# Kernel optimization log

Measured on AMD Instinct MI355X. Metric: run time of the kernel, lower is better.

The kernel has to match this reference:

```python
import jax, jax.numpy as jnp
import numpy as np
from jax import lax

N = 5000          # num atoms
E = 4             # num edge types
DIM_H = 128
VOCAB = 100       # num_atoms_vocab; embedding table has VOCAB+1 rows
T = 4             # max_time_steps


def setup_inputs() -> dict:
    key = jax.random.key(0)
    k1, k2, k3, k4 = jax.random.split(key, 4)
    atom_arr = jax.random.randint(k1, (N,), 0, VOCAB, dtype=jnp.int64 if jax.config.read('jax_enable_x64') else jnp.int32)
    adjs = jax.random.randint(k2, (E, N, N), 0, 2, dtype=jnp.int32)
    # learned parameters
    embedding = jax.random.normal(k3, (VOCAB + 1, DIM_H), dtype=jnp.float32) * 0.05
    limit = float(np.sqrt(6.0 / (DIM_H + DIM_H)))  # glorot uniform
    H_edges = jax.random.uniform(k4, (E, DIM_H, DIM_H), minval=-limit, maxval=limit, dtype=jnp.float32)
    return {
        "atom_arr": atom_arr,
        "adjs": adjs,
        "max_time_steps": T,
        "embedding": embedding,
        "H_edges": H_edges,
    }


def reference(atom_arr, adjs, max_time_steps, embedding, H_edges):
    # h_v^0 = embedding lookup, [N, H]
    h0 = embedding[atom_arr]
    # adjacency mask as float, [E, N, N]
    A = (adjs == 1).astype(h0.dtype)

    def step(h, _):
        # original: for each node v, edge type e: H_e @ sum_{u: adj[e,v,u]==1} h_u
        agg = jnp.einsum('evu,uh->evh', A, h)          # neighbor sum per edge type
        msg = jnp.einsum('eij,evj->vi', H_edges, agg)  # edge-type transform + sum over e
        h_new = jax.nn.sigmoid(h + msg)
        return h_new, h_new

    _, h_all = lax.scan(step, h0, None, length=max_time_steps)
    return h_all  # [T, N, H]
```

## Files before the change

kernel.cpp:

```cpp
#include <hip/hip_runtime.h>

#define NROW 5000
#define NPAD 5120
#define KPAD 5120
#define KW   80
#define KC   80
#define KZ   4
#define KCQ  20
#define HDIM 128
#define FXS  4194304.0f
#define PART ((size_t)4 * NROW * HDIM)

typedef _Float16 f16x8 __attribute__((ext_vector_type(8)));
typedef float f32x16 __attribute__((ext_vector_type(16)));

__device__ __forceinline__ unsigned short f2h_int(int v) {
    union { _Float16 h; unsigned short u; } c;
    c.h = (_Float16)(float)v;
    return c.u;
}
__device__ __forceinline__ void fx_digits(float h, unsigned short& d1, unsigned short& d0) {
    int q = (int)rintf(h * FXS);
    d1 = f2h_int(q >> 11);
    d0 = f2h_int(q & 2047);
}

__device__ __forceinline__ size_t ht_idx(int pl, int kc, int i, int kin) {
    return (((size_t)pl * KC + kc) * HDIM + i) * 64 + kin;
}

__global__ __launch_bounds__(256) void prep_atom_kernel(const unsigned int* __restrict__ atomw,
                                                        int* __restrict__ atomIdx) {
    __shared__ int s_is64;
    if (threadIdx.x == 0) {
        bool all0 = true, anynz = false;
        for (int j = 0; j < 64; ++j) {
            unsigned lo = atomw[2 * j], hi = atomw[2 * j + 1];
            all0 = all0 && (hi == 0u);
            anynz = anynz || (lo != 0u);
        }
        s_is64 = (all0 && anynz) ? 1 : 0;
    }
    __syncthreads();
    int v = blockIdx.x * 256 + threadIdx.x;
    if (v < NROW) atomIdx[v] = s_is64 ? (int)atomw[2 * v] : (int)atomw[v];
}

__global__ __launch_bounds__(256) void prep_pack_kernel(const int* __restrict__ adjs,
                                                        unsigned long long* __restrict__ packed) {
    const int er = blockIdx.x;
    const int e = er / NPAD;
    const int r = er - e * NPAD;
    const int wave = threadIdx.x >> 6;
    const int lane = threadIdx.x & 63;
    const int* rowp = adjs + ((size_t)e * NROW + r) * NROW;
    unsigned long long* outp = packed + ((size_t)e * NPAD + r) * KW;
    const bool rok = (r < NROW);
    for (int c = wave; c < KW; c += 4) {
        int u = c * 64 + lane;
        int val = (rok && u < NROW) ? rowp[u] : 0;
        unsigned long long m = __ballot(val == 1);
        if (lane == 0) outp[c] = m;
    }
}

__global__ __launch_bounds__(256) void prep_h0T_kernel(const int* __restrict__ atomIdx,
                                                       const float* __restrict__ emb,
                                                       unsigned short* __restrict__ hTt) {
    const int i = blockIdx.y;
    const int v = blockIdx.x * 256 + threadIdx.x;
    float val = 0.f;
    if (v < NROW) val = emb[(size_t)atomIdx[v] * HDIM + i];
    unsigned short d1, d0;
    fx_digits(val, d1, d0);
    hTt[ht_idx(0, v >> 6, i, v & 63)] = d1;
    hTt[ht_idx(1, v >> 6, i, v & 63)] = d0;
}

__global__ __launch_bounds__(256) void prep_h0f_kernel(const int* __restrict__ atomIdx,
                                                       const float* __restrict__ emb,
                                                       float* __restrict__ h) {
    int idx = blockIdx.x * 256 + threadIdx.x;
    int v = idx >> 7, i = idx & 127;
    h[idx] = emb[(size_t)atomIdx[v] * HDIM + i];
}

__global__ __launch_bounds__(256) void prep_Ht_kernel(const float* __restrict__ H,
                                                      float* __restrict__ Htr) {
    int idx = blockIdx.x * 256 + threadIdx.x;
    int e = idx >> 14;
    int j = (idx >> 7) & 127;
    int i = idx & 127;
    Htr[idx] = H[((size_t)e * HDIM + i) * HDIM + j];
}

__global__ __launch_bounds__(256, 2) void gemm1_kernel(const uint2* __restrict__ packed2,
                                                       const unsigned short* __restrict__ hTt,
                                                       float* __restrict__ agg) {
    const int m0 = blockIdx.x * 128;
    const int e = blockIdx.y;
    const int kz = blockIdx.z;
    const int tid = threadIdx.x;
    const int lane = tid & 63;
    const int wave = tid >> 6;
    const int l31 = lane & 31;
    const int l1 = lane >> 5;
    const int sh2 = l1 * 8;
    const int cb = wave * 32;
    const int col = cb + l31;

    f32x16 acc[2][4];
#pragma unroll
    for (int pl = 0; pl < 2; ++pl)
#pragma unroll
        for (int mt = 0; mt < 4; ++mt) acc[pl][mt] = (f32x16)(0.f);

    const uint2* ap[4];
#pragma unroll
    for (int mt = 0; mt < 4; ++mt)
        ap[mt] = packed2 + ((size_t)e * NPAD + (m0 + mt * 32 + l31)) * KW;

    const _Float16* bbase = (const _Float16*)hTt;
    const int kc0 = kz * KCQ;
    const _Float16* bp[2];
#pragma unroll
    for (int pl = 0; pl < 2; ++pl)
        bp[pl] = bbase + (((size_t)pl * KC + kc0) * HDIM + col) * 64 + sh2;

    for (int kc = kc0; kc < kc0 + KCQ; ++kc) {
        uint2 aw[4];
#pragma unroll
        for (int mt = 0; mt < 4; ++mt) aw[mt] = ap[mt][kc];
        const size_t coff = (size_t)(kc - kc0) * (HDIM * 64);

        f16x8 bf[2][4];
#pragma unroll
        for (int pl = 0; pl < 2; ++pl)
#pragma unroll
            for (int kk = 0; kk < 4; ++kk)
                bf[pl][kk] = *(const f16x8*)(bp[pl] + coff + kk * 16);

#pragma unroll
        for (int kk = 0; kk < 4; ++kk) {
#pragma unroll
            for (int mt = 0; mt < 4; ++mt) {
                unsigned int w = (kk < 2) ? aw[mt].x : aw[mt].y;
                unsigned int b = (w >> ((kk & 1) * 16 + sh2)) & 0xFFu;
                unsigned int y = b | (b << 15);
                union { unsigned int u[4]; f16x8 h; } A;
#pragma unroll
                for (int q = 0; q < 4; ++q)
                    A.u[q] = ((y >> (2 * q)) & 0x00010001u) * 0x3C00u;
#pragma unroll
                for (int pl = 0; pl < 2; ++pl)
                    acc[pl][mt] = __builtin_amdgcn_mfma_f32_32x32x16_f16(
                        A.h, bf[pl][kk], acc[pl][mt], 0, 0, 0);
            }
        }
    }

    float* aggz = agg + (size_t)kz * PART;
#pragma unroll
    for (int mt = 0; mt < 4; ++mt)
#pragma unroll
        for (int reg = 0; reg < 16; ++reg) {
            int row = (reg & 3) + 8 * (reg >> 2) + 4 * l1;
            int v = m0 + mt * 32 + row;
            if (v < NROW) {
                double d = (double)acc[0][mt][reg] * 2048.0 + (double)acc[1][mt][reg];
                aggz[((size_t)e * NROW + v) * HDIM + col] = (float)(d * (1.0 / 4194304.0));
            }
        }
}

__global__ __launch_bounds__(256) void gemm2_kernel(const float* __restrict__ agg,
                                                    const float* __restrict__ Htr,
                                                    float* __restrict__ h,
                                                    float* __restrict__ outp,
                                                    unsigned short* __restrict__ hTt) {
    __shared__ float aggs[16][512];
    __shared__ unsigned short hs[2][128][16];
    const int v0 = blockIdx.x * 16;
    const int tid = threadIdx.x;

#pragma unroll
    for (int it = 0; it < 8; ++it) {
        int idx = it * 256 + tid;
        int vv = idx >> 7;
        int ej = (idx & 127) * 4;
        int e = ej >> 7, j = ej & 127;
        int v = v0 + vv;
        float4 val = make_float4(0.f, 0.f, 0.f, 0.f);
        if (v < NROW) {
            size_t o = ((size_t)e * NROW + v) * HDIM + j;
            float4 a0 = *(const float4*)&agg[o];
            float4 a1 = *(const float4*)&agg[PART + o];
            float4 a2 = *(const float4*)&agg[2 * PART + o];
            float4 a3 = *(const float4*)&agg[3 * PART + o];
            val = make_float4((a0.x + a1.x) + (a2.x + a3.x), (a0.y + a1.y) + (a2.y + a3.y),
                              (a0.z + a1.z) + (a2.z + a3.z), (a0.w + a1.w) + (a2.w + a3.w));
        }
        *(float4*)&aggs[vv][ej] = val;
    }
    __syncthreads();

    const int i = tid & 127;
    const int vg = tid >> 7;
    float m4[8][4];
#pragma unroll
    for (int vv = 0; vv < 8; ++vv)
#pragma unroll
        for (int k = 0; k < 4; ++k) m4[vv][k] = 0.f;

    for (int c = 0; c < 512; c += 4) {
        float w0 = Htr[(size_t)(c + 0) * HDIM + i];
        float w1 = Htr[(size_t)(c + 1) * HDIM + i];
        float w2 = Htr[(size_t)(c + 2) * HDIM + i];
        float w3 = Htr[(size_t)(c + 3) * HDIM + i];
#pragma unroll
        for (int vv = 0; vv < 8; ++vv) {
            const float4 a = *(const float4*)&aggs[vg * 8 + vv][c];
            m4[vv][0] += a.x * w0;
            m4[vv][1] += a.y * w1;
            m4[vv][2] += a.z * w2;
            m4[vv][3] += a.w * w3;
        }
    }

#pragma unroll
    for (int vv = 0; vv < 8; ++vv) {
        int v = v0 + vg * 8 + vv;
        unsigned short d1 = 0, d0 = 0;
        if (v < NROW) {
            size_t o = (size_t)v * HDIM + i;
            float msg = (m4[vv][0] + m4[vv][1]) + (m4[vv][2] + m4[vv][3]);
            float x = h[o] + msg;
            float s = 1.0f / (1.0f + expf(-x));
            outp[o] = s;
            h[o] = s;
            fx_digits(s, d1, d0);
        }
        hs[0][i][vg * 8 + vv] = d1;
        hs[1][i][vg * 8 + vv] = d0;
    }
    __syncthreads();
    if (tid < 128) {
#pragma unroll
        for (int pl = 0; pl < 2; ++pl) {
            uint4* d = (uint4*)&hTt[ht_idx(pl, v0 >> 6, tid, v0 & 63)];
            const uint4* sp = (const uint4*)&hs[pl][tid][0];
            d[0] = sp[0];
            d[1] = sp[1];
        }
    }
}

extern "C" void kernel_launch(void* const* d_in, const int* in_sizes, int n_in,
                              void* d_out, int out_size, void* d_ws, size_t ws_size,
                              hipStream_t stream) {
    const unsigned int* atomw = (const unsigned int*)d_in[0];
    const int* adjs = (const int*)d_in[1];
    const float* emb = (const float*)d_in[3];
    const float* H = (const float*)d_in[4];
    float* out = (float*)d_out;

    char* ws = (char*)d_ws;
    unsigned long long* packed = (unsigned long long*)ws;
    size_t off = (size_t)4 * NPAD * KW * 8;
    unsigned short* hTt = (unsigned short*)(ws + off);
    off += (size_t)2 * KC * HDIM * 64 * 2;
    float* hf = (float*)(ws + off);
    off += (size_t)NROW * HDIM * 4;
    float* agg = (float*)(ws + off);
    off += (size_t)KZ * PART * 4;
    float* Htr = (float*)(ws + off);
    off += (size_t)4 * HDIM * HDIM * 4;
    int* atomIdx = (int*)(ws + off);
    off += (size_t)NROW * 4;

    prep_atom_kernel<<<dim3((NROW + 255) / 256), 256, 0, stream>>>(atomw, atomIdx);
    prep_pack_kernel<<<dim3(4 * NPAD), 256, 0, stream>>>(adjs, packed);
    prep_h0T_kernel<<<dim3(KPAD / 256, HDIM), 256, 0, stream>>>(atomIdx, emb, hTt);
    prep_h0f_kernel<<<dim3(NROW * HDIM / 256), 256, 0, stream>>>(atomIdx, emb, hf);
    prep_Ht_kernel<<<dim3(4 * HDIM * HDIM / 256), 256, 0, stream>>>(H, Htr);

    for (int t = 0; t < 4; ++t) {
        gemm1_kernel<<<dim3(NPAD / 128, 4, KZ), 256, 0, stream>>>((const uint2*)packed, hTt, agg);
        gemm2_kernel<<<dim3((NROW + 15) / 16), 256, 0, stream>>>(agg, Htr, hf,
                                                                 out + (size_t)t * NROW * HDIM, hTt);
    }
}
```

Baseline: 1.094 ms.

## Transpose packed adjacency and reorder h fragments for coalesced gemm1 loads

```diff
diff --git a/kernel.cpp b/kernel.cpp
--- a/kernel.cpp
+++ b/kernel.cpp
@@ -25,8 +25,8 @@
     d0 = f2h_int(q & 2047);
 }
 
-__device__ __forceinline__ size_t ht_idx(int pl, int kc, int i, int kin) {
-    return (((size_t)pl * KC + kc) * HDIM + i) * 64 + kin;
+__device__ __forceinline__ size_t bidx(int pl, int kc, int kk, int l1, int col, int j) {
+    return (((((size_t)pl * KC + kc) * 4 + kk) * 2 + l1) * 128 + col) * 8 + j;
 }
 
 __global__ __launch_bounds__(256) void prep_atom_kernel(const unsigned int* __restrict__ atomw,
@@ -47,20 +47,19 @@
 }
 
 __global__ __launch_bounds__(256) void prep_pack_kernel(const int* __restrict__ adjs,
-                                                        unsigned long long* __restrict__ packed) {
+                                                        unsigned long long* __restrict__ packT) {
     const int er = blockIdx.x;
     const int e = er / NPAD;
     const int r = er - e * NPAD;
     const int wave = threadIdx.x >> 6;
     const int lane = threadIdx.x & 63;
     const int* rowp = adjs + ((size_t)e * NROW + r) * NROW;
-    unsigned long long* outp = packed + ((size_t)e * NPAD + r) * KW;
     const bool rok = (r < NROW);
     for (int c = wave; c < KW; c += 4) {
         int u = c * 64 + lane;
         int val = (rok && u < NROW) ? rowp[u] : 0;
         unsigned long long m = __ballot(val == 1);
-        if (lane == 0) outp[c] = m;
+        if (lane == 0) packT[((size_t)e * KW + c) * NPAD + r] = m;
     }
 }
 
@@ -73,8 +72,9 @@
     if (v < NROW) val = emb[(size_t)atomIdx[v] * HDIM + i];
     unsigned short d1, d0;
     fx_digits(val, d1, d0);
-    hTt[ht_idx(0, v >> 6, i, v & 63)] = d1;
-    hTt[ht_idx(1, v >> 6, i, v & 63)] = d0;
+    const int kc = v >> 6, kk = (v >> 4) & 3, l1 = (v >> 3) & 1, j = v & 7;
+    hTt[bidx(0, kc, kk, l1, i, j)] = d1;
+    hTt[bidx(1, kc, kk, l1, i, j)] = d0;
 }
 
 __global__ __launch_bounds__(256) void prep_h0f_kernel(const int* __restrict__ atomIdx,
@@ -94,7 +94,7 @@
     Htr[idx] = H[((size_t)e * HDIM + i) * HDIM + j];
 }
 
-__global__ __launch_bounds__(256, 2) void gemm1_kernel(const uint2* __restrict__ packed2,
+__global__ __launch_bounds__(256, 2) void gemm1_kernel(const unsigned long long* __restrict__ packT,
                                                        const unsigned short* __restrict__ hTt,
                                                        float* __restrict__ agg) {
     const int m0 = blockIdx.x * 128;
@@ -115,30 +115,27 @@
 #pragma unroll
         for (int mt = 0; mt < 4; ++mt) acc[pl][mt] = (f32x16)(0.f);
 
-    const uint2* ap[4];
-#pragma unroll
-    for (int mt = 0; mt < 4; ++mt)
-        ap[mt] = packed2 + ((size_t)e * NPAD + (m0 + mt * 32 + l31)) * KW;
-
+    const int kc0 = kz * KCQ;
     const _Float16* bbase = (const _Float16*)hTt;
-    const int kc0 = kz * KCQ;
     const _Float16* bp[2];
 #pragma unroll
     for (int pl = 0; pl < 2; ++pl)
-        bp[pl] = bbase + (((size_t)pl * KC + kc0) * HDIM + col) * 64 + sh2;
+        bp[pl] = bbase + bidx(pl, kc0, 0, l1, col, 0);
 
     for (int kc = kc0; kc < kc0 + KCQ; ++kc) {
+        const unsigned long long* arow = packT + ((size_t)e * KW + kc) * NPAD + m0 + l31;
         uint2 aw[4];
 #pragma unroll
-        for (int mt = 0; mt < 4; ++mt) aw[mt] = ap[mt][kc];
-        const size_t coff = (size_t)(kc - kc0) * (HDIM * 64);
-
+        for (int mt = 0; mt < 4; ++mt)
+            aw[mt] = ((const uint2*)arow)[mt * 32];
+
+        const size_t coff = (size_t)(kc - kc0) * 8192;
         f16x8 bf[2][4];
 #pragma unroll
         for (int pl = 0; pl < 2; ++pl)
 #pragma unroll
             for (int kk = 0; kk < 4; ++kk)
-                bf[pl][kk] = *(const f16x8*)(bp[pl] + coff + kk * 16);
+                bf[pl][kk] = *(const f16x8*)(bp[pl] + coff + (size_t)kk * 2048);
 
 #pragma unroll
         for (int kk = 0; kk < 4; ++kk) {
@@ -245,13 +242,14 @@
     }
     __syncthreads();
     if (tid < 128) {
-#pragma unroll
-        for (int pl = 0; pl < 2; ++pl) {
-            uint4* d = (uint4*)&hTt[ht_idx(pl, v0 >> 6, tid, v0 & 63)];
-            const uint4* sp = (const uint4*)&hs[pl][tid][0];
-            d[0] = sp[0];
-            d[1] = sp[1];
-        }
+        const int kc = v0 >> 6, kk = (v0 >> 4) & 3;
+#pragma unroll
+        for (int pl = 0; pl < 2; ++pl)
+#pragma unroll
+            for (int l1 = 0; l1 < 2; ++l1) {
+                uint4* d = (uint4*)&hTt[bidx(pl, kc, kk, l1, tid, 0)];
+                *d = *(const uint4*)&hs[pl][tid][l1 * 8];
+            }
     }
 }
 
@@ -265,10 +263,10 @@
     float* out = (float*)d_out;
 
     char* ws = (char*)d_ws;
-    unsigned long long* packed = (unsigned long long*)ws;
+    unsigned long long* packT = (unsigned long long*)ws;
     size_t off = (size_t)4 * NPAD * KW * 8;
     unsigned short* hTt = (unsigned short*)(ws + off);
-    off += (size_t)2 * KC * HDIM * 64 * 2;
+    off += (size_t)2 * KC * 4 * 2 * 128 * 8 * 2;
     float* hf = (float*)(ws + off);
     off += (size_t)NROW * HDIM * 4;
     float* agg = (float*)(ws + off);
@@ -279,13 +277,13 @@
     off += (size_t)NROW * 4;
 
     prep_atom_kernel<<<dim3((NROW + 255) / 256), 256, 0, stream>>>(atomw, atomIdx);
-    prep_pack_kernel<<<dim3(4 * NPAD), 256, 0, stream>>>(adjs, packed);
+    prep_pack_kernel<<<dim3(4 * NPAD), 256, 0, stream>>>(adjs, packT);
     prep_h0T_kernel<<<dim3(KPAD / 256, HDIM), 256, 0, stream>>>(atomIdx, emb, hTt);
     prep_h0f_kernel<<<dim3(NROW * HDIM / 256), 256, 0, stream>>>(atomIdx, emb, hf);
     prep_Ht_kernel<<<dim3(4 * HDIM * HDIM / 256), 256, 0, stream>>>(H, Htr);
 
     for (int t = 0; t < 4; ++t) {
-        gemm1_kernel<<<dim3(NPAD / 128, 4, KZ), 256, 0, stream>>>((const uint2*)packed, hTt, agg);
+        gemm1_kernel<<<dim3(NPAD / 128, 4, KZ), 256, 0, stream>>>(packT, hTt, agg);
         gemm2_kernel<<<dim3((NROW + 15) / 16), 256, 0, stream>>>(agg, Htr, hf,
                                                                  out + (size_t)t * NROW * HDIM, hTt);
     }
```

Result: slower. 1.120 ms (+2.4%).
